# Optimization experiments

Measured on AMD Instinct MI355X. Metric: run time of the kernel, lower is better.

## Reference

```python
import jax, jax.numpy as jnp
import numpy as np

IMAGE_W = IMAGE_H = 608
TOP_N = 1000
MIN_SCORE = 0.05
NMS_THR = 0.5
MAX_DET = 100
B = 8
NUM_CLASSES = 80
STRIDES = [32, 16, 8]
ANCHOR_WH = {32: [[116, 90], [156, 198], [373, 326]],
             16: [[30, 61], [62, 45], [59, 119]],
             8: [[10, 13], [16, 30], [33, 23]]}


def _make_anchors(stride):
    # anchors layout [B,g,g,3,5] = (grid_x, grid_y, anchor_w*stride, anchor_h*stride, stride)
    g = IMAGE_W // stride
    ys, xs = jnp.meshgrid(jnp.arange(g, dtype=jnp.float32),
                          jnp.arange(g, dtype=jnp.float32), indexing='ij')
    grid = jnp.broadcast_to(jnp.stack([xs, ys], -1)[:, :, None, :], (g, g, 3, 2))
    wh = jnp.asarray(ANCHOR_WH[stride], dtype=jnp.float32) * stride
    wh = jnp.broadcast_to(wh[None, None, :, :], (g, g, 3, 2))
    s = jnp.full((g, g, 3, 1), float(stride), dtype=jnp.float32)
    a = jnp.concatenate([grid, wh, s], -1)
    return jnp.broadcast_to(a[None], (B, g, g, 3, 5))


def setup_inputs() -> dict:
    key = jax.random.key(0)
    ks = jax.random.split(key, 9)
    inp = {}
    for i, stride in enumerate(STRIDES):
        g = IMAGE_W // stride
        inp[f'obj{i}'] = jax.random.normal(ks[3 * i + 0], (B, g, g, 3, 1), jnp.float32)
        inp[f'reg{i}'] = jax.random.normal(ks[3 * i + 1], (B, g, g, 3, 4), jnp.float32)
        inp[f'cls{i}'] = jax.random.normal(ks[3 * i + 2], (B, g, g, 3, NUM_CLASSES), jnp.float32)
        inp[f'anchors{i}'] = _make_anchors(stride)
    return inp


def _decode_level(obj, reg, cls, anch):
    Bn = obj.shape[0]
    obj = jax.nn.sigmoid(obj.reshape(Bn, -1))                       # [B,N]
    cls = jax.nn.sigmoid(cls.reshape(Bn, -1, cls.shape[-1]))        # [B,N,C]
    reg = reg.reshape(Bn, -1, 4)
    anch = anch.reshape(Bn, -1, 5)
    ctr = (jax.nn.sigmoid(reg[..., 0:2]) + anch[..., 0:2]) * anch[..., 4:5]
    wh = jnp.exp(reg[..., 2:4]) * anch[..., 2:4] / anch[..., 4:5]
    x1y1 = ctr - 0.5 * wh
    x2y2 = wh + x1y1
    boxes = jnp.concatenate([x1y1, x2y2], -1).astype(jnp.int32)     # trunc toward zero == torch .int()
    boxes = jnp.stack([jnp.maximum(boxes[..., 0], 0),
                       jnp.maximum(boxes[..., 1], 0),
                       jnp.minimum(boxes[..., 2], IMAGE_W - 1),
                       jnp.minimum(boxes[..., 3], IMAGE_H - 1)], -1)
    scores = jnp.max(cls, axis=-1) * obj
    classes = jnp.argmax(cls, axis=-1).astype(jnp.int32)
    if scores.shape[1] >= TOP_N:
        scores, idx = jax.lax.top_k(scores, TOP_N)
        classes = jnp.take_along_axis(classes, idx, axis=1)
        boxes = jnp.take_along_axis(boxes, idx[..., None], axis=1)
    return scores, classes, boxes


def _nms_one_image(scores, classes, boxes):
    # scores [N], classes int32 [N], boxes int32 [N,4]
    N = scores.shape[0]
    valid = scores > MIN_SCORE
    s = jnp.where(valid, scores, -1.0)
    order = jnp.argsort(-s)
    s = s[order]
    valid = valid[order]
    cls_f = classes[order].astype(jnp.float32)
    b = boxes[order].astype(jnp.float32)
    areas = (b[:, 2] - b[:, 0]) * (b[:, 3] - b[:, 1])
    idxs = jnp.arange(N)

    def body(i, keep):
        box = b[i]
        xx1 = jnp.maximum(box[0], b[:, 0])
        yy1 = jnp.maximum(box[1], b[:, 1])
        xx2 = jnp.minimum(box[2], b[:, 2])
        yy2 = jnp.minimum(box[3], b[:, 3])
        inter = jnp.maximum(xx2 - xx1, 0.0) * jnp.maximum(yy2 - yy1, 0.0)
        iou = inter / (areas[i] + areas - inter)
        suppress = keep[i] & (idxs > i) & (iou > NMS_THR)
        return keep & ~suppress

    keep = jax.lax.fori_loop(0, N, body, valid)
    pos = jnp.cumsum(keep) - 1                       # output slot of each kept box
    slot = jnp.where(keep & (pos < MAX_DET), pos, MAX_DET)  # overflow/dropped -> dump slot
    out_s = jnp.full((MAX_DET + 1,), -1.0, jnp.float32).at[slot].set(s)[:MAX_DET]
    out_c = jnp.full((MAX_DET + 1,), -1.0, jnp.float32).at[slot].set(cls_f)[:MAX_DET]
    out_b = jnp.full((MAX_DET + 1, 4), -1.0, jnp.float32).at[slot].set(b)[:MAX_DET]
    return out_s, out_c, out_b


def _forward(obj0, obj1, obj2, reg0, reg1, reg2, cls0, cls1, cls2,
             anchors0, anchors1, anchors2):
    objs = [obj0, obj1, obj2]
    regs = [reg0, reg1, reg2]
    clss = [cls0, cls1, cls2]
    anchs = [anchors0, anchors1, anchors2]
    sc, cl, bx = [], [], []
    for o, r, c, a in zip(objs, regs, clss, anchs):
        s_, c_, b_ = _decode_level(o, r, c, a)
        sc.append(s_); cl.append(c_); bx.append(b_)
    scores = jnp.concatenate(sc, axis=1)
    classes = jnp.concatenate(cl, axis=1)
    boxes = jnp.concatenate(bx, axis=1)
    return jax.vmap(_nms_one_image)(scores, classes, boxes)


def reference(obj0, obj1, obj2, reg0, reg1, reg2, cls0, cls1, cls2,
              anchors0, anchors1, anchors2):
    return _forward(obj0, obj1, obj2, reg0, reg1, reg2, cls0, cls1, cls2,
                    anchors0, anchors1, anchors2)
```

## Files before the change

### kernel.cpp

```cpp
#include <hip/hip_runtime.h>
#include <math.h>

constexpr int BATCH   = 8;
constexpr int NUM_CLS = 80;
constexpr int N0 = 19 * 19 * 3;
constexpr int N1 = 38 * 38 * 3;
constexpr int N2 = 76 * 76 * 3;
constexpr int OFF1 = N0;
constexpr int OFF2 = N0 + N1;
constexpr int NTOT = N0 + N1 + N2;
constexpr int TOPN = 1000;
constexpr int NSEL = 3 * TOPN;
constexpr int MAXDET = 100;
constexpr float MIN_SCORE_F = 0.05f;
constexpr int IMG_MAX = 607;

__device__ __forceinline__ float sigmoidf_(float x) {
    return 1.0f / (1.0f + expf(-x));
}

__constant__ float AWH[3][3][2] = {
    {{116.f, 90.f}, {156.f, 198.f}, {373.f, 326.f}},
    {{ 30.f, 61.f}, { 62.f,  45.f}, { 59.f, 119.f}},
    {{ 10.f, 13.f}, { 16.f,  30.f}, { 33.f,  23.f}},
};

__device__ __forceinline__ bool iou_gt(float4 a, float4 c) {
    float ai = (a.z - a.x) * (a.w - a.y);
    float aj = (c.z - c.x) * (c.w - c.y);
    float xx1 = fmaxf(a.x, c.x);
    float yy1 = fmaxf(a.y, c.y);
    float xx2 = fminf(a.z, c.z);
    float yy2 = fminf(a.w, c.w);
    float inter = fmaxf(xx2 - xx1, 0.0f) * fmaxf(yy2 - yy1, 0.0f);
    float uni = ai + aj - inter;
    return (inter > 0.5f * uni) && (inter > 0.0f);
}

__global__ __launch_bounds__(256) void k_decode(
    const float* __restrict__ obj0, const float* __restrict__ reg0,
    const float* __restrict__ cls0,
    const float* __restrict__ obj1, const float* __restrict__ reg1,
    const float* __restrict__ cls1,
    const float* __restrict__ obj2, const float* __restrict__ reg2,
    const float* __restrict__ cls2,
    unsigned long long* __restrict__ decKey, float* __restrict__ decC,
    float* __restrict__ decB, int* __restrict__ gflagImg, int* __restrict__ fbCursor)
{
    if (blockIdx.x == 0 && threadIdx.x < 32) {
        if (threadIdx.x < 8)  gflagImg[threadIdx.x] = 0;
        if (threadIdx.x < 24) fbCursor[threadIdx.x] = 0;
    }

    __shared__ float sBest[64];
    __shared__ int   sCls[64];

    int g0 = blockIdx.x * 64;
    int t  = threadIdx.x;

    {
        int q  = t >> 2;
        int lq = t & 3;
        int idx = g0 + q;
        if (idx < BATCH * NTOT) {
            int b  = idx / NTOT;
            int na = idx - b * NTOT;
            const float* cls; int Nl, n;
            if (na < OFF1)      { cls = cls0; Nl = N0; n = na; }
            else if (na < OFF2) { cls = cls1; Nl = N1; n = na - OFF1; }
            else                { cls = cls2; Nl = N2; n = na - OFF2; }
            size_t bn = (size_t)b * Nl + n;

            const float4* cv = reinterpret_cast<const float4*>(cls + bn * NUM_CLS);
            float best = -1.0f; int bc = 0;
            #pragma unroll
            for (int k = 0; k < 5; ++k) {
                int m = lq + 4 * k;
                float4 v = cv[m];
                float s;
                s = sigmoidf_(v.x); if (s > best) { best = s; bc = 4 * m + 0; }
                s = sigmoidf_(v.y); if (s > best) { best = s; bc = 4 * m + 1; }
                s = sigmoidf_(v.z); if (s > best) { best = s; bc = 4 * m + 2; }
                s = sigmoidf_(v.w); if (s > best) { best = s; bc = 4 * m + 3; }
            }
            #pragma unroll
            for (int d = 1; d <= 2; d <<= 1) {
                float ob = __shfl_xor(best, d);
                int   oc = __shfl_xor(bc, d);
                if (ob > best || (ob == best && oc < bc)) { best = ob; bc = oc; }
            }
            if (lq == 0) { sBest[q] = best; sCls[q] = bc; }
        }
    }
    __syncthreads();

    if (t < 64) {
        int idx = g0 + t;
        if (idx < BATCH * NTOT) {
            int b  = idx / NTOT;
            int na = idx - b * NTOT;
            const float *obj, *reg;
            int Nl, n, lvl, g;
            float st;
            if (na < OFF1)      { obj = obj0; reg = reg0; Nl = N0; n = na;        lvl = 0; g = 19; st = 32.f; }
            else if (na < OFF2) { obj = obj1; reg = reg1; Nl = N1; n = na - OFF1; lvl = 1; g = 38; st = 16.f; }
            else                { obj = obj2; reg = reg2; Nl = N2; n = na - OFF2; lvl = 2; g = 76; st = 8.f;  }
            size_t bn = (size_t)b * Nl + n;

            float so    = sigmoidf_(obj[bn]);
            float score = sBest[t] * so;
            int   bc    = sCls[t];

            int a    = n % 3;
            int cell = n / 3;
            int gx   = cell % g;
            int gy   = cell / g;
            float ax = (float)gx, ay = (float)gy;
            float aw = AWH[lvl][a][0], ah = AWH[lvl][a][1];

            float4 rv = reinterpret_cast<const float4*>(reg)[bn];
            float cx = (sigmoidf_(rv.x) + ax) * st;
            float cy = (sigmoidf_(rv.y) + ay) * st;
            float w  = expf(rv.z) * aw;
            float h  = expf(rv.w) * ah;
            float x1f = cx - 0.5f * w;
            float y1f = cy - 0.5f * h;
            float x2f = w + x1f;
            float y2f = h + y1f;
            int x1 = (int)x1f, y1 = (int)y1f, x2 = (int)x2f, y2 = (int)y2f;
            x1 = (x1 < 0) ? 0 : x1;
            y1 = (y1 < 0) ? 0 : y1;
            x2 = (x2 > IMG_MAX) ? IMG_MAX : x2;
            y2 = (y2 > IMG_MAX) ? IMG_MAX : y2;

            size_t gg = (size_t)b * NTOT + na;
            decKey[gg] = ((unsigned long long)__float_as_uint(score) << 15) | (unsigned)(Nl - n);
            decC[gg] = (float)bc;
            reinterpret_cast<float4*>(decB)[gg] =
                make_float4((float)x1, (float)y1, (float)x2, (float)y2);
        }
    }
}

constexpr int NBIN  = 4096;
constexpr int STCAP = 2048;
constexpr int KPT   = 17;

__global__ __launch_bounds__(1024) void k_select(
    const unsigned long long* __restrict__ decKey, const float* __restrict__ decC,
    const float* __restrict__ decB, float* __restrict__ selS, float* __restrict__ selC,
    float* __restrict__ selB, unsigned long long* __restrict__ selKey,
    int* __restrict__ gflagImg, int* __restrict__ fbCursor)
{
    __shared__ unsigned hist[NBIN];
    __shared__ unsigned cum[NBIN];
    __shared__ unsigned wscan[32];
    __shared__ unsigned long long stKey[STCAP];
    __shared__ int stIdx[STCAP];
    __shared__ int sTot; __shared__ int sOvf;
    __shared__ int sBstar; __shared__ int sNeed;

    int b   = blockIdx.x / 3;
    int lvl = blockIdx.x % 3;
    int off = (lvl == 0) ? 0 : (lvl == 1) ? OFF1 : OFF2;
    int Nl  = (lvl == 0) ? N0 : (lvl == 1) ? N1 : N2;
    int tid = threadIdx.x;
    int lane = tid & 63;
    int wv   = tid >> 6;

    const unsigned long long* keys = decKey + (size_t)b * NTOT + off;

    unsigned long long kk[KPT];
    #pragma unroll
    for (int i = 0; i < KPT; ++i) {
        int t = tid + i * 1024;
        kk[i] = (t < Nl) ? keys[t] : 0ull;
    }

    for (int t = tid; t < NBIN; t += 1024) hist[t] = 0;
    if (tid == 0) { sTot = 0; sOvf = 0; }
    __syncthreads();

    #pragma unroll
    for (int i = 0; i < KPT; ++i) {
        int t = tid + i * 1024;
        if (t < Nl) atomicAdd(&hist[(unsigned)(kk[i] >> 33)], 1u);
    }
    __syncthreads();

    {
        uint4 hh = reinterpret_cast<uint4*>(hist)[tid];
        reinterpret_cast<uint4*>(hist)[tid] = make_uint4(0u, 0u, 0u, 0u);
        unsigned ssum = hh.x + hh.y + hh.z + hh.w;

        unsigned sfx = ssum;
        #pragma unroll
        for (int d = 1; d < 64; d <<= 1) {
            unsigned o = __shfl_down(sfx, d);
            if (lane + d < 64) sfx += o;
        }
        if (lane == 0) wscan[wv] = sfx;
        __syncthreads();
        if (tid < 16) {
            unsigned v = wscan[tid];
            unsigned s2 = v;
            #pragma unroll
            for (int d = 1; d < 16; d <<= 1) {
                unsigned o = __shfl_down(s2, d);
                if (tid + d < 16) s2 += o;
            }
            wscan[16 + tid] = s2 - v;
        }
        __syncthreads();
        unsigned Tt = wscan[16 + wv] + (sfx - ssum);
        unsigned c3 = Tt;
        unsigned c2 = c3 + hh.w;
        unsigned c1 = c2 + hh.z;
        unsigned c0 = c1 + hh.y;
        reinterpret_cast<uint4*>(cum)[tid] = make_uint4(c0, c1, c2, c3);
    }
    __syncthreads();

    #pragma unroll
    for (int i = 0; i < KPT; ++i) {
        int t = tid + i * 1024;
        if (t < Nl) {
            unsigned long long k = kk[i];
            unsigned bin = (unsigned)(k >> 33);
            if (cum[bin] < (unsigned)TOPN) {
                unsigned c = atomicAdd(&hist[bin], 1u);
                unsigned p = cum[bin] + c;
                if (p < STCAP) { stKey[p] = k; stIdx[p] = t; }
                else sOvf = 1;
            }
        }
    }
    __syncthreads();

    {
        uint4 hh = reinterpret_cast<uint4*>(hist)[tid];
        uint4 cc = reinterpret_cast<uint4*>(cum)[tid];
        unsigned loc = 0;
        if (cc.x < (unsigned)TOPN) loc += hh.x;
        if (cc.y < (unsigned)TOPN) loc += hh.y;
        if (cc.z < (unsigned)TOPN) loc += hh.z;
        if (cc.w < (unsigned)TOPN) loc += hh.w;
        #pragma unroll
        for (int d = 1; d < 64; d <<= 1) loc += __shfl_down(loc, d);
        if (lane == 0 && loc) atomicAdd(&sTot, (int)loc);
    }
    __syncthreads();

    auto writeOut = [&](int t, int r) {
        size_t g = (size_t)b * NTOT + off + t;
        unsigned long long k = keys[t];
        float sraw = __uint_as_float((unsigned)(k >> 15));
        float strn = (sraw > MIN_SCORE_F) ? sraw : -1.0f;
        int G = off + t;
        unsigned long long gk =
            ((unsigned long long)(__float_as_uint(sraw) | 0x80000000u) << 16) |
            (unsigned)(NTOT - G);
        int o = b * NSEL + lvl * TOPN + r;
        selS[o] = strn;
        selC[o] = decC[g];
        selKey[o] = gk;
        reinterpret_cast<float4*>(selB)[o] = reinterpret_cast<const float4*>(decB)[g];
    };

    if (sOvf == 0) {
        int M = sTot;
        for (int p = tid; p < M; p += 1024) {
            unsigned long long k = stKey[p];
            unsigned bin = (unsigned)(k >> 33);
            unsigned start = cum[bin], end = start + hist[bin];
            int r = (int)start;
            for (unsigned q = start; q < end; ++q) r += (stKey[q] > k) ? 1 : 0;
            if (r < TOPN) writeOut(stIdx[p], r);
        }
    } else {
        if (tid == 0) {
            gflagImg[b] = 1;
            int B = 0;
            for (int bin = NBIN - 1; bin >= 0; --bin) {
                if (cum[bin] <= (unsigned)(TOPN - 1) &&
                    cum[bin] + hist[bin] > (unsigned)(TOPN - 1)) { B = bin; break; }
            }
            sBstar = B; sNeed = TOPN - (int)cum[B];
        }
        __syncthreads();
        int Bstar = sBstar, need = sNeed;
        for (int t = tid; t < Nl; t += 1024) {
            unsigned long long k = keys[t];
            int bin = (int)(unsigned)(k >> 33);
            bool em = false;
            if (bin > Bstar) em = true;
            else if (bin == Bstar) {
                int r = 0;
                for (int j = 0; j < Nl; ++j) {
                    unsigned long long kj = keys[j];
                    r += ((int)(unsigned)(kj >> 33) == Bstar && kj > k) ? 1 : 0;
                }
                em = (r < need);
            }
            if (em) {
                int r = atomicAdd(&fbCursor[b * 3 + lvl], 1);
                writeOut(t, r);
            }
        }
    }
}

constexpr int NPT = 3;

__global__ __launch_bounds__(1024) void k_nms(
    const float* __restrict__ selS, const float* __restrict__ selC,
    const float* __restrict__ selB, const unsigned long long* __restrict__ selKey,
    const int* __restrict__ gflagImg,
    float* __restrict__ out)
{
    __shared__ union {
        unsigned long long keys[NSEL];
        float4 boxes[NSEL];
    } U;
    __shared__ int ord[NSEL];
    __shared__ float4 keptBox[MAXDET];
    __shared__ int keptRank[MAXDET];
    __shared__ int sPos; __shared__ int sNValid;

    int b = blockIdx.x, tid = threadIdx.x;
    const float* S = selS + b * NSEL;

    float sv[NPT];
    {
        unsigned long long kv[NPT];
        #pragma unroll
        for (int i = 0; i < NPT; ++i) {
            int t = tid + i * 1024;
            kv[i] = (t < NSEL) ? selKey[b * NSEL + t] : 0ull;
            sv[i] = (t < NSEL) ? S[t] : -1.0f;
        }
        #pragma unroll
        for (int i = 0; i < NPT; ++i) {
            int t = tid + i * 1024;
            if (t < NSEL) U.keys[t] = kv[i];
        }
    }
    if (tid == 0) sNValid = 0;
    __syncthreads();
    int fb = gflagImg[b];

    int myR[NPT];
    int nvLoc = 0;
    #pragma unroll
    for (int i = 0; i < NPT; ++i) {
        int t = tid + i * 1024;
        myR[i] = -1;
        if (t < NSEL) {
            unsigned long long k = U.keys[t];
            int rank;
            if (!fb) {
                int l = t / TOPN;
                rank = t - l * TOPN;
                #pragma unroll
                for (int m = 0; m < 3; ++m) {
                    if (m == l) continue;
                    int base = m * TOPN, lo = 0, hi = TOPN;
                    while (lo < hi) {
                        int mid = (lo + hi) >> 1;
                        if (U.keys[base + mid] > k) lo = mid + 1; else hi = mid;
                    }
                    rank += lo;
                }
            } else {
                int r = 0;
                for (int j = 0; j < NSEL; ++j) r += (U.keys[j] > k) ? 1 : 0;
                rank = r;
            }
            myR[i] = rank;
            if (sv[i] > MIN_SCORE_F) nvLoc++;
        }
    }
    #pragma unroll
    for (int d = 1; d < 64; d <<= 1) nvLoc += __shfl_down(nvLoc, d);
    if ((tid & 63) == 0 && nvLoc) atomicAdd(&sNValid, nvLoc);
    __syncthreads();

    {
        float4 bb[NPT];
        #pragma unroll
        for (int i = 0; i < NPT; ++i) {
            int t = tid + i * 1024;
            bb[i] = (t < NSEL) ? reinterpret_cast<const float4*>(selB)[b * NSEL + t]
                               : make_float4(0.f, 0.f, 0.f, 0.f);
        }
        #pragma unroll
        for (int i = 0; i < NPT; ++i) {
            int t = tid + i * 1024;
            if (t < NSEL) { U.boxes[myR[i]] = bb[i]; ord[myR[i]] = t; }
        }
    }
    __syncthreads();

    if (tid < 64) {
        int lane = tid;
        int nValid = sNValid;
        int pos = 0;
        int nW = (nValid + 63) >> 6;
        for (int w = 0; w < nW && pos < MAXDET; ++w) {
            int j = w * 64 + lane;
            float4 bx = (j < NSEL) ? U.boxes[j]
                                   : make_float4(4e8f, 4e8f, -4e8f, -4e8f);
            bool valid = (j < nValid);
            bool sup = false;
            for (int q = 0; q < pos; ++q)
                sup = sup || iou_gt(keptBox[q], bx);
            unsigned long long live = __ballot(valid && !sup);
            while (live) {
                int p = __ffsll(live) - 1;
                if (lane == 0) keptRank[pos] = w * 64 + p;
                if (lane == p) keptBox[pos] = bx;
                pos++;
                if (pos >= MAXDET) break;
                float kx = __shfl(bx.x, p), ky = __shfl(bx.y, p);
                float kz = __shfl(bx.z, p), kw = __shfl(bx.w, p);
                bool hit = iou_gt(make_float4(kx, ky, kz, kw), bx);
                live &= ~__ballot(hit);
                live &= ~(1ull << p);
            }
        }
        if (lane == 0) sPos = pos;
    }
    __syncthreads();

    int pos = sPos;
    const float* C = selC + b * NSEL;
    float* out_s = out + b * MAXDET;
    float* out_c = out + BATCH * MAXDET + b * MAXDET;
    float* out_b = out + 2 * BATCH * MAXDET + (size_t)b * MAXDET * 4;
    for (int t = tid; t < MAXDET; t += 1024) {
        if (t < pos) {
            int i = keptRank[t];
            int o = ord[i];
            float4 bb = U.boxes[i];
            out_s[t] = S[o];
            out_c[t] = C[o];
            out_b[t * 4 + 0] = bb.x; out_b[t * 4 + 1] = bb.y;
            out_b[t * 4 + 2] = bb.z; out_b[t * 4 + 3] = bb.w;
        } else {
            out_s[t] = -1.0f; out_c[t] = -1.0f;
            out_b[t * 4 + 0] = -1.0f; out_b[t * 4 + 1] = -1.0f;
            out_b[t * 4 + 2] = -1.0f; out_b[t * 4 + 3] = -1.0f;
        }
    }
}

extern "C" void kernel_launch(void* const* d_in, const int* in_sizes, int n_in,
                              void* d_out, int out_size, void* d_ws, size_t ws_size,
                              hipStream_t stream) {
    (void)n_in; (void)out_size; (void)ws_size;

    bool dict = (in_sizes[2] == BATCH * N0 * NUM_CLS);
    const float *obj[3], *reg[3], *cls[3];
    for (int l = 0; l < 3; ++l) {
        obj[l] = (const float*)d_in[dict ? 4 * l + 0 : l];
        reg[l] = (const float*)d_in[dict ? 4 * l + 1 : 3 + l];
        cls[l] = (const float*)d_in[dict ? 4 * l + 2 : 6 + l];
    }

    char* ws = (char*)d_ws;
    size_t off = 0;
    auto take = [&](size_t bytes) -> void* {
        void* p = ws + off;
        off += (bytes + 255) & ~(size_t)255;
        return p;
    };
    int*                 gflagImg = (int*)take(BATCH * sizeof(int));
    int*                 fbCursor = (int*)take(BATCH * 3 * sizeof(int));
    unsigned long long*  decKey   = (unsigned long long*)take((size_t)BATCH * NTOT * 8);
    float*               decC     = (float*)take((size_t)BATCH * NTOT * 4);
    float*               decB     = (float*)take((size_t)BATCH * NTOT * 16);
    float*               selS     = (float*)take((size_t)BATCH * NSEL * 4);
    float*               selC     = (float*)take((size_t)BATCH * NSEL * 4);
    float*               selB     = (float*)take((size_t)BATCH * NSEL * 16);
    unsigned long long*  selKey   = (unsigned long long*)take((size_t)BATCH * NSEL * 8);

    int totalDec = BATCH * NTOT;
    k_decode<<<(totalDec + 63) / 64, 256, 0, stream>>>(
        obj[0], reg[0], cls[0],
        obj[1], reg[1], cls[1],
        obj[2], reg[2], cls[2],
        decKey, decC, decB, gflagImg, fbCursor);

    k_select<<<BATCH * 3, 1024, 0, stream>>>(decKey, decC, decB,
                                             selS, selC, selB, selKey,
                                             gflagImg, fbCursor);

    k_nms<<<BATCH, 1024, 0, stream>>>(selS, selC, selB, selKey, gflagImg,
                                      (float*)d_out);
}
```

Before: 168.2 us.

## Defer box decode to selected candidates and pack class into sort key

Box regression decoding moves from the full-anchor decode kernel into the top-N selection kernel, so boxes are computed only for the up to 1000 selected candidates per level instead of every anchor. The class index is packed into the low bits of the 64-bit score key, and the score is recovered from the key. This removes the intermediate decC/decB/selS/selC buffers and their global writes and reads. The cost is extra bit-packing logic, with key layout and shifts changed across all three kernels, and the reg reads for selected candidates become scattered gathers.

```diff
diff --git a/kernel.cpp b/kernel.cpp
--- a/kernel.cpp
+++ b/kernel.cpp
@@ -38,14 +38,11 @@
 }
 
 __global__ __launch_bounds__(256) void k_decode(
-    const float* __restrict__ obj0, const float* __restrict__ reg0,
-    const float* __restrict__ cls0,
-    const float* __restrict__ obj1, const float* __restrict__ reg1,
-    const float* __restrict__ cls1,
-    const float* __restrict__ obj2, const float* __restrict__ reg2,
-    const float* __restrict__ cls2,
-    unsigned long long* __restrict__ decKey, float* __restrict__ decC,
-    float* __restrict__ decB, int* __restrict__ gflagImg, int* __restrict__ fbCursor)
+    const float* __restrict__ obj0, const float* __restrict__ cls0,
+    const float* __restrict__ obj1, const float* __restrict__ cls1,
+    const float* __restrict__ obj2, const float* __restrict__ cls2,
+    unsigned long long* __restrict__ decKey,
+    int* __restrict__ gflagImg, int* __restrict__ fbCursor)
 {
     if (blockIdx.x == 0 && threadIdx.x < 32) {
         if (threadIdx.x < 8)  gflagImg[threadIdx.x] = 0;
@@ -99,45 +96,21 @@
         if (idx < BATCH * NTOT) {
             int b  = idx / NTOT;
             int na = idx - b * NTOT;
-            const float *obj, *reg;
-            int Nl, n, lvl, g;
-            float st;
-            if (na < OFF1)      { obj = obj0; reg = reg0; Nl = N0; n = na;        lvl = 0; g = 19; st = 32.f; }
-            else if (na < OFF2) { obj = obj1; reg = reg1; Nl = N1; n = na - OFF1; lvl = 1; g = 38; st = 16.f; }
-            else                { obj = obj2; reg = reg2; Nl = N2; n = na - OFF2; lvl = 2; g = 76; st = 8.f;  }
+            const float* obj;
+            int Nl, n;
+            if (na < OFF1)      { obj = obj0; Nl = N0; n = na;        }
+            else if (na < OFF2) { obj = obj1; Nl = N1; n = na - OFF1; }
+            else                { obj = obj2; Nl = N2; n = na - OFF2; }
             size_t bn = (size_t)b * Nl + n;
 
             float so    = sigmoidf_(obj[bn]);
             float score = sBest[t] * so;
             int   bc    = sCls[t];
 
-            int a    = n % 3;
-            int cell = n / 3;
-            int gx   = cell % g;
-            int gy   = cell / g;
-            float ax = (float)gx, ay = (float)gy;
-            float aw = AWH[lvl][a][0], ah = AWH[lvl][a][1];
-
-            float4 rv = reinterpret_cast<const float4*>(reg)[bn];
-            float cx = (sigmoidf_(rv.x) + ax) * st;
-            float cy = (sigmoidf_(rv.y) + ay) * st;
-            float w  = expf(rv.z) * aw;
-            float h  = expf(rv.w) * ah;
-            float x1f = cx - 0.5f * w;
-            float y1f = cy - 0.5f * h;
-            float x2f = w + x1f;
-            float y2f = h + y1f;
-            int x1 = (int)x1f, y1 = (int)y1f, x2 = (int)x2f, y2 = (int)y2f;
-            x1 = (x1 < 0) ? 0 : x1;
-            y1 = (y1 < 0) ? 0 : y1;
-            x2 = (x2 > IMG_MAX) ? IMG_MAX : x2;
-            y2 = (y2 > IMG_MAX) ? IMG_MAX : y2;
-
             size_t gg = (size_t)b * NTOT + na;
-            decKey[gg] = ((unsigned long long)__float_as_uint(score) << 15) | (unsigned)(Nl - n);
-            decC[gg] = (float)bc;
-            reinterpret_cast<float4*>(decB)[gg] =
-                make_float4((float)x1, (float)y1, (float)x2, (float)y2);
+            decKey[gg] = ((unsigned long long)__float_as_uint(score) << 22)
+                       | ((unsigned long long)(unsigned)(Nl - n) << 7)
+                       | (unsigned)bc;
         }
     }
 }
@@ -147,8 +120,9 @@
 constexpr int KPT   = 17;
 
 __global__ __launch_bounds__(1024) void k_select(
-    const unsigned long long* __restrict__ decKey, const float* __restrict__ decC,
-    const float* __restrict__ decB, float* __restrict__ selS, float* __restrict__ selC,
+    const unsigned long long* __restrict__ decKey,
+    const float* __restrict__ reg0, const float* __restrict__ reg1,
+    const float* __restrict__ reg2,
     float* __restrict__ selB, unsigned long long* __restrict__ selKey,
     int* __restrict__ gflagImg, int* __restrict__ fbCursor)
 {
@@ -164,6 +138,9 @@
     int lvl = blockIdx.x % 3;
     int off = (lvl == 0) ? 0 : (lvl == 1) ? OFF1 : OFF2;
     int Nl  = (lvl == 0) ? N0 : (lvl == 1) ? N1 : N2;
+    int gsz = (lvl == 0) ? 19 : (lvl == 1) ? 38 : 76;
+    float st = (lvl == 0) ? 32.f : (lvl == 1) ? 16.f : 8.f;
+    const float* reg = (lvl == 0) ? reg0 : (lvl == 1) ? reg1 : reg2;
     int tid = threadIdx.x;
     int lane = tid & 63;
     int wv   = tid >> 6;
@@ -184,7 +161,7 @@
     #pragma unroll
     for (int i = 0; i < KPT; ++i) {
         int t = tid + i * 1024;
-        if (t < Nl) atomicAdd(&hist[(unsigned)(kk[i] >> 33)], 1u);
+        if (t < Nl) atomicAdd(&hist[(unsigned)(kk[i] >> 42)], 1u);
     }
     __syncthreads();
 
@@ -226,7 +203,7 @@
         int t = tid + i * 1024;
         if (t < Nl) {
             unsigned long long k = kk[i];
-            unsigned bin = (unsigned)(k >> 33);
+            unsigned bin = (unsigned)(k >> 42);
             if (cum[bin] < (unsigned)TOPN) {
                 unsigned c = atomicAdd(&hist[bin], 1u);
                 unsigned p = cum[bin] + c;
@@ -251,31 +228,51 @@
     }
     __syncthreads();
 
-    auto writeOut = [&](int t, int r) {
-        size_t g = (size_t)b * NTOT + off + t;
-        unsigned long long k = keys[t];
-        float sraw = __uint_as_float((unsigned)(k >> 15));
-        float strn = (sraw > MIN_SCORE_F) ? sraw : -1.0f;
+    auto writeOut = [&](int t, int r, unsigned long long k) {
+        float sraw = __uint_as_float((unsigned)(k >> 22));
+        int   bc   = (int)(k & 0x7F);
         int G = off + t;
         unsigned long long gk =
-            ((unsigned long long)(__float_as_uint(sraw) | 0x80000000u) << 16) |
-            (unsigned)(NTOT - G);
+            (((unsigned long long)(__float_as_uint(sraw) | 0x80000000u)) << 23) |
+            ((unsigned long long)(unsigned)(NTOT - G) << 7) | (unsigned)bc;
+
+        size_t bn = (size_t)b * Nl + t;
+        float4 rv = reinterpret_cast<const float4*>(reg)[bn];
+        int a    = t % 3;
+        int cell = t / 3;
+        int gx   = cell % gsz;
+        int gy   = cell / gsz;
+        float ax = (float)gx, ay = (float)gy;
+        float aw = AWH[lvl][a][0], ah = AWH[lvl][a][1];
+        float cx = (sigmoidf_(rv.x) + ax) * st;
+        float cy = (sigmoidf_(rv.y) + ay) * st;
+        float w  = expf(rv.z) * aw;
+        float h  = expf(rv.w) * ah;
+        float x1f = cx - 0.5f * w;
+        float y1f = cy - 0.5f * h;
+        float x2f = w + x1f;
+        float y2f = h + y1f;
+        int x1 = (int)x1f, y1 = (int)y1f, x2 = (int)x2f, y2 = (int)y2f;
+        x1 = (x1 < 0) ? 0 : x1;
+        y1 = (y1 < 0) ? 0 : y1;
+        x2 = (x2 > IMG_MAX) ? IMG_MAX : x2;
+        y2 = (y2 > IMG_MAX) ? IMG_MAX : y2;
+
         int o = b * NSEL + lvl * TOPN + r;
-        selS[o] = strn;
-        selC[o] = decC[g];
         selKey[o] = gk;
-        reinterpret_cast<float4*>(selB)[o] = reinterpret_cast<const float4*>(decB)[g];
+        reinterpret_cast<float4*>(selB)[o] =
+            make_float4((float)x1, (float)y1, (float)x2, (float)y2);
     };
 
     if (sOvf == 0) {
         int M = sTot;
         for (int p = tid; p < M; p += 1024) {
             unsigned long long k = stKey[p];
-            unsigned bin = (unsigned)(k >> 33);
+            unsigned bin = (unsigned)(k >> 42);
             unsigned start = cum[bin], end = start + hist[bin];
             int r = (int)start;
             for (unsigned q = start; q < end; ++q) r += (stKey[q] > k) ? 1 : 0;
-            if (r < TOPN) writeOut(stIdx[p], r);
+            if (r < TOPN) writeOut(stIdx[p], r, k);
         }
     } else {
         if (tid == 0) {
@@ -291,20 +288,20 @@
         int Bstar = sBstar, need = sNeed;
         for (int t = tid; t < Nl; t += 1024) {
             unsigned long long k = keys[t];
-            int bin = (int)(unsigned)(k >> 33);
+            int bin = (int)(unsigned)(k >> 42);
             bool em = false;
             if (bin > Bstar) em = true;
             else if (bin == Bstar) {
                 int r = 0;
                 for (int j = 0; j < Nl; ++j) {
                     unsigned long long kj = keys[j];
-                    r += ((int)(unsigned)(kj >> 33) == Bstar && kj > k) ? 1 : 0;
+                    r += ((int)(unsigned)(kj >> 42) == Bstar && kj > k) ? 1 : 0;
                 }
                 em = (r < need);
             }
             if (em) {
                 int r = atomicAdd(&fbCursor[b * 3 + lvl], 1);
-                writeOut(t, r);
+                writeOut(t, r, k);
             }
         }
     }
@@ -313,7 +310,6 @@
 constexpr int NPT = 3;
 
 __global__ __launch_bounds__(1024) void k_nms(
-    const float* __restrict__ selS, const float* __restrict__ selC,
     const float* __restrict__ selB, const unsigned long long* __restrict__ selKey,
     const int* __restrict__ gflagImg,
     float* __restrict__ out)
@@ -328,16 +324,17 @@
     __shared__ int sPos; __shared__ int sNValid;
 
     int b = blockIdx.x, tid = threadIdx.x;
-    const float* S = selS + b * NSEL;
-
-    float sv[NPT];
+    const unsigned bits05 = __float_as_uint(MIN_SCORE_F);
+
+    bool vld[NPT];
     {
         unsigned long long kv[NPT];
         #pragma unroll
         for (int i = 0; i < NPT; ++i) {
             int t = tid + i * 1024;
             kv[i] = (t < NSEL) ? selKey[b * NSEL + t] : 0ull;
-            sv[i] = (t < NSEL) ? S[t] : -1.0f;
+            vld[i] = (t < NSEL) &&
+                     (((unsigned)(kv[i] >> 23) & 0x7FFFFFFFu) > bits05);
         }
         #pragma unroll
         for (int i = 0; i < NPT; ++i) {
@@ -377,7 +374,7 @@
                 rank = r;
             }
             myR[i] = rank;
-            if (sv[i] > MIN_SCORE_F) nvLoc++;
+            if (vld[i]) nvLoc++;
         }
     }
     #pragma unroll
@@ -433,7 +430,6 @@
     __syncthreads();
 
     int pos = sPos;
-    const float* C = selC + b * NSEL;
     float* out_s = out + b * MAXDET;
     float* out_c = out + BATCH * MAXDET + b * MAXDET;
     float* out_b = out + 2 * BATCH * MAXDET + (size_t)b * MAXDET * 4;
@@ -441,9 +437,12 @@
         if (t < pos) {
             int i = keptRank[t];
             int o = ord[i];
+            unsigned long long gk = selKey[b * NSEL + o];
+            float sraw = __uint_as_float((unsigned)(gk >> 23) & 0x7FFFFFFFu);
+            float clsf = (float)(int)(gk & 0x7F);
             float4 bb = U.boxes[i];
-            out_s[t] = S[o];
-            out_c[t] = C[o];
+            out_s[t] = sraw;
+            out_c[t] = clsf;
             out_b[t * 4 + 0] = bb.x; out_b[t * 4 + 1] = bb.y;
             out_b[t * 4 + 2] = bb.z; out_b[t * 4 + 3] = bb.w;
         } else {
@@ -477,24 +476,20 @@
     int*                 gflagImg = (int*)take(BATCH * sizeof(int));
     int*                 fbCursor = (int*)take(BATCH * 3 * sizeof(int));
     unsigned long long*  decKey   = (unsigned long long*)take((size_t)BATCH * NTOT * 8);
-    float*               decC     = (float*)take((size_t)BATCH * NTOT * 4);
-    float*               decB     = (float*)take((size_t)BATCH * NTOT * 16);
-    float*               selS     = (float*)take((size_t)BATCH * NSEL * 4);
-    float*               selC     = (float*)take((size_t)BATCH * NSEL * 4);
     float*               selB     = (float*)take((size_t)BATCH * NSEL * 16);
     unsigned long long*  selKey   = (unsigned long long*)take((size_t)BATCH * NSEL * 8);
 
     int totalDec = BATCH * NTOT;
     k_decode<<<(totalDec + 63) / 64, 256, 0, stream>>>(
-        obj[0], reg[0], cls[0],
-        obj[1], reg[1], cls[1],
-        obj[2], reg[2], cls[2],
-        decKey, decC, decB, gflagImg, fbCursor);
-
-    k_select<<<BATCH * 3, 1024, 0, stream>>>(decKey, decC, decB,
-                                             selS, selC, selB, selKey,
+        obj[0], cls[0],
+        obj[1], cls[1],
+        obj[2], cls[2],
+        decKey, gflagImg, fbCursor);
+
+    k_select<<<BATCH * 3, 1024, 0, stream>>>(decKey, reg[0], reg[1], reg[2],
+                                             selB, selKey,
                                              gflagImg, fbCursor);
 
-    k_nms<<<BATCH, 1024, 0, stream>>>(selS, selC, selB, selKey, gflagImg,
+    k_nms<<<BATCH, 1024, 0, stream>>>(selB, selKey, gflagImg,
                                       (float*)d_out);
 }
```

Measured after the change: 185.3 us. +10.2%, slower.
